# Optimization experiments

Measured on AMD Instinct MI355X. Metric: run time of the kernel, lower is better.

Reference implementation:

```python
import jax, jax.numpy as jnp
import numpy as np

N_EMBD = 1024
N_HEAD = 16
LORA_R = 8
LORA_ALPHA = 16
SCALE = LORA_ALPHA / LORA_R


def lora_linear(x, W, b, A, Bm):
    # loralib: F.linear(x, W, b) + (x @ A.T @ B.T) * scaling
    return x @ W.T + b + ((x @ A.T) @ Bm.T) * SCALE


def setup_inputs() -> dict:
    key = jax.random.key(0)
    ks = jax.random.split(key, 9)
    B, T, C = 4, 2048, N_EMBD
    s_in = 1.0 / np.sqrt(C)
    x = jax.random.normal(ks[0], (B, T, C), dtype=jnp.float32)
    Wqkv = jax.random.normal(ks[1], (3 * C, C), dtype=jnp.float32) * s_in
    bqkv = jnp.zeros((3 * C,), dtype=jnp.float32)
    Aqkv = jax.random.normal(ks[2], (LORA_R, C), dtype=jnp.float32) * s_in
    Bqkv = jnp.zeros((3 * C, LORA_R), dtype=jnp.float32)  # loralib inits B to zero
    Wproj = jax.random.normal(ks[3], (C, C), dtype=jnp.float32) * s_in
    bproj = jnp.zeros((C,), dtype=jnp.float32)
    Aproj = jax.random.normal(ks[4], (LORA_R, C), dtype=jnp.float32) * s_in
    Bproj = jnp.zeros((C, LORA_R), dtype=jnp.float32)
    return {"x": x, "Wqkv": Wqkv, "bqkv": bqkv, "Aqkv": Aqkv, "Bqkv": Bqkv,
            "Wproj": Wproj, "bproj": bproj, "Aproj": Aproj, "Bproj": Bproj}


def reference(x, Wqkv, bqkv, Aqkv, Bqkv, Wproj, bproj, Aproj, Bproj):
    B, T, C = x.shape
    H, D = N_HEAD, C // N_HEAD
    qkv = lora_linear(x, Wqkv, bqkv, Aqkv, Bqkv)  # [B,T,3C]
    q, k, v = jnp.split(qkv, 3, axis=2)
    # [B,T,C] -> [B,H,T,D]
    q = q.reshape(B, T, H, D).transpose(0, 2, 1, 3)
    k = k.reshape(B, T, H, D).transpose(0, 2, 1, 3)
    v = v.reshape(B, T, H, D).transpose(0, 2, 1, 3)
    att = jnp.einsum("bhqd,bhkd->bhqk", q, k) * (1.0 / np.sqrt(D))
    causal = jnp.tril(jnp.ones((T, T), dtype=bool))
    att = jnp.where(causal[None, None], att, jnp.float32(-jnp.inf))
    att = jax.nn.softmax(att, axis=-1)
    out = jnp.einsum("bhqk,bhkd->bhqd", att, v)  # [B,H,T,D]
    out = out.transpose(0, 2, 1, 3).reshape(B, T, C)
    return lora_linear(out, Wproj, bproj, Aproj, Bproj)
```

## Files before the change

kernel.cpp:

```cpp
#include <hip/hip_runtime.h>
#include <hip/hip_bf16.h>

typedef __bf16 bf16_t;
typedef __bf16 bf16x8 __attribute__((ext_vector_type(8)));
typedef __bf16 bf16x4 __attribute__((ext_vector_type(4)));
typedef float  f32x4  __attribute__((ext_vector_type(4)));

#define MFMA_BF16 __builtin_amdgcn_mfma_f32_16x16x32_bf16
#define NEG_BIG  (-3.0e38f)

#if __has_builtin(__builtin_amdgcn_exp2f)
#define EXP2F(x) __builtin_amdgcn_exp2f(x)
#else
#define EXP2F(x) exp2f(x)
#endif

#define SBAR()       __builtin_amdgcn_s_barrier()
#define SCHED0()     __builtin_amdgcn_sched_barrier(0)
#define WAIT_LGKM0() asm volatile("s_waitcnt lgkmcnt(0)" ::: "memory")
#define WAIT_LGKM8() asm volatile("s_waitcnt lgkmcnt(8)" ::: "memory")
#define WAIT_VM0()   asm volatile("s_waitcnt vmcnt(0)" ::: "memory")
#define WAIT_VM4()   asm volatile("s_waitcnt vmcnt(4)" ::: "memory")
#define WAIT_VM6()   asm volatile("s_waitcnt vmcnt(6)" ::: "memory")

__device__ __forceinline__ void load16_lds(const bf16_t* g, bf16_t* l) {
    __builtin_amdgcn_global_load_lds(
        (const __attribute__((address_space(1))) void*)g,
        (__attribute__((address_space(3))) void*)l, 16, 0, 0);
}

__device__ inline bf16x8 ld8(const bf16_t* p) { return *(const bf16x8*)p; }
__device__ inline bf16x8 ld8(const float* p) {
    f32x4 a = *(const f32x4*)p;
    f32x4 b = *(const f32x4*)(p + 4);
    bf16x8 o;
    o[0] = (bf16_t)a[0]; o[1] = (bf16_t)a[1]; o[2] = (bf16_t)a[2]; o[3] = (bf16_t)a[3];
    o[4] = (bf16_t)b[0]; o[5] = (bf16_t)b[1]; o[6] = (bf16_t)b[2]; o[7] = (bf16_t)b[3];
    return o;
}

template <typename TX>
__device__ __forceinline__ void lora_xa_body(
    const TX* __restrict__ X, const float* __restrict__ A,
    float* __restrict__ out, int m, int lane)
{
    const TX* xp = X + (size_t)m * 1024;
    float acc[8];
#pragma unroll
    for (int r = 0; r < 8; r++) acc[r] = 0.f;

#pragma unroll 4
    for (int ci = 0; ci < 16; ci++) {
        int k = ci * 64 + lane;
        float xv = (float)xp[k];
#pragma unroll
        for (int r = 0; r < 8; r++) acc[r] += xv * A[r * 1024 + k];
    }
#pragma unroll
    for (int r = 0; r < 8; r++) {
        float v = acc[r];
        v += __shfl_xor(v, 1);  v += __shfl_xor(v, 2);  v += __shfl_xor(v, 4);
        v += __shfl_xor(v, 8);  v += __shfl_xor(v, 16); v += __shfl_xor(v, 32);
        if (lane == 0) out[m * 8 + r] = v;
    }
}

template <typename TX>
__global__ __launch_bounds__(256) void lora_xa_kernel(
    const TX* __restrict__ X, const float* __restrict__ A,
    float* __restrict__ out)
{
    const int lane = threadIdx.x & 63;
    const int w    = threadIdx.x >> 6;
    const int m    = blockIdx.x * 4 + w;
    lora_xa_body<TX>(X, A, out, m, lane);
}

__global__ __launch_bounds__(256) void prep_kernel(
    const float* __restrict__ x, const float* __restrict__ Wqkv,
    const float* __restrict__ Wproj,
    bf16_t* __restrict__ x16, bf16_t* __restrict__ Wqkv16,
    bf16_t* __restrict__ Wproj16,
    const float* __restrict__ Aqkv, float* __restrict__ xa1)
{
    const int bid = blockIdx.x;
    if (bid < 6144) {
        const float* in; bf16_t* out; size_t off;
        if (bid < 4096)      { in = x;     out = x16;     off = (size_t)bid * 2048; }
        else if (bid < 5632) { in = Wqkv;  out = Wqkv16;  off = (size_t)(bid - 4096) * 2048; }
        else                 { in = Wproj; out = Wproj16; off = (size_t)(bid - 5632) * 2048; }
        size_t i = off + (size_t)threadIdx.x * 8;
        *(bf16x8*)&out[i] = ld8(&in[i]);
    } else {
        const int lane = threadIdx.x & 63;
        const int w    = threadIdx.x >> 6;
        const int m    = (bid - 6144) * 4 + w;
        lora_xa_body<float>(x, Aqkv, xa1, m, lane);
    }
}

__device__ __forceinline__ void gemm_epilogue(
    f32x4 (&acc)[4][4], const float* bias, const float* xA, const float* LB,
    bf16_t* C0, bf16_t* C1, bf16_t* C2, float* Cf,
    int tile_m, int tile_n, int wm, int wn, int c, int g)
{
    const int seg    = tile_n >> 10;
    const int tn_loc = tile_n & 1023;
    bf16_t* Cout = (seg == 0) ? C0 : (seg == 1) ? C1 : C2;

    float biasf[4];
    float lbv[4][8];
#pragma unroll
    for (int j = 0; j < 4; j++) {
        int col = tile_n + wn + j * 16 + c;
        biasf[j] = bias[col];
        f32x4 lb0 = *(const f32x4*)&LB[(size_t)col * 8];
        f32x4 lb1 = *(const f32x4*)&LB[(size_t)col * 8 + 4];
#pragma unroll
        for (int r = 0; r < 4; r++) { lbv[j][r] = lb0[r]; lbv[j][r + 4] = lb1[r]; }
    }
#pragma unroll
    for (int i = 0; i < 4; i++) {
#pragma unroll
        for (int rg = 0; rg < 4; rg++) {
            int row = tile_m + wm + i * 16 + g * 4 + rg;
            f32x4 xa0 = *(const f32x4*)&xA[(size_t)row * 8];
            f32x4 xa1 = *(const f32x4*)&xA[(size_t)row * 8 + 4];
#pragma unroll
            for (int j = 0; j < 4; j++) {
                float lora = xa0[0] * lbv[j][0] + xa0[1] * lbv[j][1] +
                             xa0[2] * lbv[j][2] + xa0[3] * lbv[j][3] +
                             xa1[0] * lbv[j][4] + xa1[1] * lbv[j][5] +
                             xa1[2] * lbv[j][6] + xa1[3] * lbv[j][7];
                float v = acc[i][j][rg] + biasf[j] + 2.0f * lora;
                int lcol = tn_loc + wn + j * 16 + c;
                if (Cf) Cf[(size_t)row * 1024 + lcol] = v;
                else    Cout[(size_t)row * 1024 + lcol] = (bf16_t)v;
            }
        }
    }
}

template <typename TA, typename TW>
__global__ __launch_bounds__(256) void gemm_bias_lora(
    const TA* __restrict__ A, const TW* __restrict__ W,
    const float* __restrict__ bias, const float* __restrict__ xA,
    const float* __restrict__ LB,
    bf16_t* __restrict__ C0, bf16_t* __restrict__ C1, bf16_t* __restrict__ C2,
    float* __restrict__ Cf, int K)
{
    __shared__ __align__(16) bf16_t As[128 * 72];
    __shared__ __align__(16) bf16_t Bs[128 * 72];

    const int t    = threadIdx.x;
    const int lane = t & 63;
    const int w    = t >> 6;
    const int wm   = (w >> 1) * 64;
    const int wn   = (w & 1) * 64;
    const int c    = lane & 15;
    const int g    = lane >> 4;
    const int tile_m = blockIdx.y * 128;
    const int tile_n = blockIdx.x * 128;

    const int srow = t >> 3;
    const int scol = (t & 7) * 8;

    f32x4 acc[4][4];
#pragma unroll
    for (int i = 0; i < 4; i++)
#pragma unroll
        for (int j = 0; j < 4; j++) {
            f32x4 z = {0.f, 0.f, 0.f, 0.f};
            acc[i][j] = z;
        }

    for (int k0 = 0; k0 < K; k0 += 64) {
#pragma unroll
        for (int i = 0; i < 4; i++) {
            int r = srow + i * 32;
            *(bf16x8*)&As[r * 72 + scol] = ld8(&A[(size_t)(tile_m + r) * K + k0 + scol]);
            *(bf16x8*)&Bs[r * 72 + scol] = ld8(&W[(size_t)(tile_n + r) * K + k0 + scol]);
        }
        __syncthreads();

#pragma unroll
        for (int kk = 0; kk < 2; kk++) {
            bf16x8 af[4], bfr[4];
#pragma unroll
            for (int i = 0; i < 4; i++)
                af[i] = *(const bf16x8*)&As[(wm + i * 16 + c) * 72 + kk * 32 + g * 8];
#pragma unroll
            for (int j = 0; j < 4; j++)
                bfr[j] = *(const bf16x8*)&Bs[(wn + j * 16 + c) * 72 + kk * 32 + g * 8];
#pragma unroll
            for (int i = 0; i < 4; i++)
#pragma unroll
                for (int j = 0; j < 4; j++)
                    acc[i][j] = MFMA_BF16(af[i], bfr[j], acc[i][j], 0, 0, 0);
        }
        __syncthreads();
    }
    gemm_epilogue(acc, bias, xA, LB, C0, C1, C2, Cf, tile_m, tile_n, wm, wn, c, g);
}

#define AS_OFF(row, q) ((row) * 64 + (((q) ^ ((row) & 7)) * 8))

__global__ __launch_bounds__(256) void gemm_proj_fused(
    const bf16_t* __restrict__ A, const bf16_t* __restrict__ W,
    const float* __restrict__ bias, const float* __restrict__ Ap,
    const float* __restrict__ LB, float* __restrict__ Cf, int K)
{
    __shared__ __align__(16) bf16_t As[128 * 64];
    __shared__ __align__(16) bf16_t Bs[128 * 64];
    __shared__ __align__(16) bf16_t Ap16[8 * 1032];

    const int t    = threadIdx.x;
    const int lane = t & 63;
    const int w    = t >> 6;
    const int wm   = (w >> 1) * 64;
    const int wn   = (w & 1) * 64;
    const int c    = lane & 15;
    const int g    = lane >> 4;
    const int tile_m = blockIdx.y * 128;
    const int tile_n = blockIdx.x * 128;

    {
        int r = t >> 5;
        int k = (t & 31) * 32;
        const float* src = Ap + (size_t)r * 1024 + k;
        bf16_t* dst = &Ap16[r * 1032 + k];
#pragma unroll
        for (int e = 0; e < 32; e += 8)
            *(bf16x8*)&dst[e] = ld8(&src[e]);
    }

    const int trow = t >> 3;
    const int k8   = (t & 7) ^ (trow & 7);
    const bf16_t* Ab = A + (size_t)tile_m * K + k8 * 8;
    const bf16_t* Wb = W + (size_t)tile_n * K + k8 * 8;

    f32x4 acc[4][4];
#pragma unroll
    for (int i = 0; i < 4; i++)
#pragma unroll
        for (int j = 0; j < 4; j++) {
            f32x4 z = {0.f, 0.f, 0.f, 0.f};
            acc[i][j] = z;
        }
    f32x4 accx[2];
    {
        f32x4 z = {0.f, 0.f, 0.f, 0.f};
        accx[0] = z; accx[1] = z;
    }

    for (int k0 = 0; k0 < K; k0 += 64) {
#pragma unroll
        for (int i = 0; i < 4; i++) {
            int row = i * 32 + trow;
            load16_lds(&Ab[(size_t)row * K + k0], &As[(i * 256 + t) * 8]);
            load16_lds(&Wb[(size_t)row * K + k0], &Bs[(i * 256 + t) * 8]);
        }
        __syncthreads();

#pragma unroll
        for (int kk = 0; kk < 2; kk++) {
            bf16x8 af[4], bfr[4];
#pragma unroll
            for (int i = 0; i < 4; i++)
                af[i] = *(const bf16x8*)&As[AS_OFF(wm + i * 16 + c, kk * 4 + g)];
#pragma unroll
            for (int j = 0; j < 4; j++)
                bfr[j] = *(const bf16x8*)&Bs[AS_OFF(wn + j * 16 + c, kk * 4 + g)];
#pragma unroll
            for (int i = 0; i < 4; i++)
#pragma unroll
                for (int j = 0; j < 4; j++)
                    acc[i][j] = MFMA_BF16(af[i], bfr[j], acc[i][j], 0, 0, 0);
            bf16x8 apf = *(const bf16x8*)&Ap16[(c & 7) * 1032 + k0 + kk * 32 + g * 8];
#pragma unroll
            for (int fi = 0; fi < 2; fi++) {
                bf16x8 xf = *(const bf16x8*)&As[AS_OFF(w * 32 + fi * 16 + c, kk * 4 + g)];
                accx[fi] = MFMA_BF16(xf, apf, accx[fi], 0, 0, 0);
            }
        }
        __syncthreads();
    }

    float* xa2l = (float*)As;
    if (c < 8) {
#pragma unroll
        for (int fi = 0; fi < 2; fi++)
#pragma unroll
            for (int rg = 0; rg < 4; rg++)
                xa2l[(w * 32 + fi * 16 + g * 4 + rg) * 8 + c] = accx[fi][rg];
    }
    __syncthreads();

    float biasf[4];
    float lbv[4][8];
#pragma unroll
    for (int j = 0; j < 4; j++) {
        int col = tile_n + wn + j * 16 + c;
        biasf[j] = bias[col];
        f32x4 lb0 = *(const f32x4*)&LB[(size_t)col * 8];
        f32x4 lb1 = *(const f32x4*)&LB[(size_t)col * 8 + 4];
#pragma unroll
        for (int r = 0; r < 4; r++) { lbv[j][r] = lb0[r]; lbv[j][r + 4] = lb1[r]; }
    }
#pragma unroll
    for (int i = 0; i < 4; i++) {
#pragma unroll
        for (int rg = 0; rg < 4; rg++) {
            int rloc = wm + i * 16 + g * 4 + rg;
            int row  = tile_m + rloc;
            f32x4 xa0 = *(const f32x4*)&xa2l[rloc * 8];
            f32x4 xa1 = *(const f32x4*)&xa2l[rloc * 8 + 4];
#pragma unroll
            for (int j = 0; j < 4; j++) {
                float lora = xa0[0] * lbv[j][0] + xa0[1] * lbv[j][1] +
                             xa0[2] * lbv[j][2] + xa0[3] * lbv[j][3] +
                             xa1[0] * lbv[j][4] + xa1[1] * lbv[j][5] +
                             xa1[2] * lbv[j][6] + xa1[3] * lbv[j][7];
                float v = acc[i][j][rg] + biasf[j] + 2.0f * lora;
                Cf[(size_t)row * 1024 + tile_n + wn + j * 16 + c] = v;
            }
        }
    }
}

__global__ __launch_bounds__(512, 2) void gemm_256(
    const bf16_t* __restrict__ A, const bf16_t* __restrict__ W,
    const float* __restrict__ bias, const float* __restrict__ xA,
    const float* __restrict__ LB,
    bf16_t* __restrict__ C0, bf16_t* __restrict__ C1, bf16_t* __restrict__ C2,
    float* __restrict__ Cf, int K, int ntn)
{
    __shared__ __align__(16) bf16_t As[4][8192];
    __shared__ __align__(16) bf16_t Bs[4][8192];

    const int t    = threadIdx.x;
    const int lane = t & 63;
    const int w    = t >> 6;
    const int c    = lane & 15;
    const int g    = lane >> 4;

    const int nwg = gridDim.x;
    const int cpx = nwg >> 3;
    const int bid = blockIdx.x;
    const int swz = (bid & 7) * cpx + (bid >> 3);
    const int tile_m = (swz / ntn) * 256;
    const int tile_n = (swz % ntn) * 256;

    const int wm  = (w >> 2) * 128;
    const int wn  = (w & 3) * 64;
    const int ha  = w >> 2;
    const int hb  = wn >> 7;
    const int wnl = wn & 127;

    int aoffs[8][2], boffs[4][2];
#pragma unroll
    for (int il = 0; il < 8; il++) {
        int rl = il * 16 + c;
#pragma unroll
        for (int ks = 0; ks < 2; ks++)
            aoffs[il][ks] = rl * 64 + (((ks * 4 + g) ^ (rl & 7)) * 8);
    }
#pragma unroll
    for (int j2 = 0; j2 < 4; j2++) {
        int rl = wnl + j2 * 16 + c;
#pragma unroll
        for (int ks = 0; ks < 2; ks++)
            boffs[j2][ks] = rl * 64 + (((ks * 4 + g) ^ (rl & 7)) * 8);
    }

    const int trow = t >> 3;
    const int qq   = (t & 7) ^ (trow & 7);
    const bf16_t* aO = A + (size_t)(tile_m + trow) * K + qq * 8;
    const bf16_t* wO = W + (size_t)(tile_n + trow) * K + qq * 8;
    const size_t rK64 = (size_t)64 * K;

#define STAGE_A(T, h) do {                                                         \
    load16_lds(aO + (size_t)(h) * 128 * K + (size_t)(T) * 64,                      \
               &As[((T) & 1) * 2 + (h)][t * 8]);                                   \
    load16_lds(aO + (size_t)(h) * 128 * K + rK64 + (size_t)(T) * 64,               \
               &As[((T) & 1) * 2 + (h)][4096 + t * 8]); } while (0)
#define STAGE_B(T, h) do {                                                         \
    load16_lds(wO + (size_t)(h) * 128 * K + (size_t)(T) * 64,                      \
               &Bs[((T) & 1) * 2 + (h)][t * 8]);                                   \
    load16_lds(wO + (size_t)(h) * 128 * K + rK64 + (size_t)(T) * 64,               \
               &Bs[((T) & 1) * 2 + (h)][4096 + t * 8]); } while (0)

    f32x4 acc[8][4];
#pragma unroll
    for (int i = 0; i < 8; i++)
#pragma unroll
        for (int j2 = 0; j2 < 4; j2++) {
            f32x4 z = {0.f, 0.f, 0.f, 0.f};
            acc[i][j2] = z;
        }

    const int NT = K >> 6;

    STAGE_B(0, 0); STAGE_B(0, 1); STAGE_A(0, 0); STAGE_A(0, 1);
    WAIT_VM4();
    STAGE_B(1, 0); STAGE_B(1, 1); STAGE_A(1, 0);
    WAIT_VM6();
    SBAR();

    for (int j = 0; j < NT; j++) {
        const bf16_t* Ab = &As[(j & 1) * 2 + ha][0];
        const bf16_t* Bb = &Bs[(j & 1) * 2 + hb][0];
        bf16x8 bfr[4][2], af0[4], af1[4];

#pragma unroll
        for (int j2 = 0; j2 < 4; j2++) {
            bfr[j2][0] = *(const bf16x8*)&Bb[boffs[j2][0]];
            bfr[j2][1] = *(const bf16x8*)&Bb[boffs[j2][1]];
        }
#pragma unroll
        for (int i = 0; i < 4; i++) af0[i] = *(const bf16x8*)&Ab[aoffs[i][0]];
        if (j + 1 < NT) STAGE_A(j + 1, 1);
        WAIT_LGKM8();
        SBAR();
        WAIT_LGKM0();
        SCHED0();
        __builtin_amdgcn_s_setprio(1);
#pragma unroll
        for (int i = 0; i < 4; i++)
#pragma unroll
            for (int j2 = 0; j2 < 4; j2++)
                acc[i][j2] = MFMA_BF16(af0[i], bfr[j2][0], acc[i][j2], 0, 0, 0);
        __builtin_amdgcn_s_setprio(0);
        SBAR();

#pragma unroll
        for (int i = 0; i < 4; i++) af1[i] = *(const bf16x8*)&Ab[aoffs[i + 4][0]];
        if (j + 2 < NT) STAGE_B(j + 2, 0);
        SBAR();
        WAIT_LGKM0();
        SCHED0();
        __builtin_amdgcn_s_setprio(1);
#pragma unroll
        for (int i = 0; i < 4; i++)
#pragma unroll
            for (int j2 = 0; j2 < 4; j2++)
                acc[4 + i][j2] = MFMA_BF16(af1[i], bfr[j2][0], acc[4 + i][j2], 0, 0, 0);
        __builtin_amdgcn_s_setprio(0);
        SBAR();

#pragma unroll
        for (int i = 0; i < 4; i++) af0[i] = *(const bf16x8*)&Ab[aoffs[i][1]];
#pragma unroll
        for (int i = 0; i < 4; i++) af1[i] = *(const bf16x8*)&Ab[aoffs[i + 4][1]];
        if (j + 2 < NT) STAGE_B(j + 2, 1);
        SBAR();
        WAIT_LGKM0();
        SCHED0();
        __builtin_amdgcn_s_setprio(1);
#pragma unroll
        for (int i = 0; i < 4; i++)
#pragma unroll
            for (int j2 = 0; j2 < 4; j2++)
                acc[i][j2] = MFMA_BF16(af0[i], bfr[j2][1], acc[i][j2], 0, 0, 0);
        __builtin_amdgcn_s_setprio(0);
        SBAR();

        if (j + 2 < NT) STAGE_A(j + 2, 0);
        SBAR();
        __builtin_amdgcn_s_setprio(1);
#pragma unroll
        for (int i = 0; i < 4; i++)
#pragma unroll
            for (int j2 = 0; j2 < 4; j2++)
                acc[4 + i][j2] = MFMA_BF16(af1[i], bfr[j2][1], acc[4 + i][j2], 0, 0, 0);
        __builtin_amdgcn_s_setprio(0);
        if (j < NT - 2) WAIT_VM6(); else WAIT_VM0();
        SBAR();
    }
#undef STAGE_A
#undef STAGE_B

    const int seg    = tile_n >> 10;
    const int tn_loc = tile_n & 1023;
    bf16_t* Cout = (seg == 0) ? C0 : (seg == 1) ? C1 : C2;

    float biasf[4];
    float lbv[4][8];
#pragma unroll
    for (int j2 = 0; j2 < 4; j2++) {
        int col = tile_n + wn + j2 * 16 + c;
        biasf[j2] = bias[col];
        f32x4 lb0 = *(const f32x4*)&LB[(size_t)col * 8];
        f32x4 lb1 = *(const f32x4*)&LB[(size_t)col * 8 + 4];
#pragma unroll
        for (int r = 0; r < 4; r++) { lbv[j2][r] = lb0[r]; lbv[j2][r + 4] = lb1[r]; }
    }
#pragma unroll
    for (int i = 0; i < 8; i++) {
#pragma unroll
        for (int rg = 0; rg < 4; rg++) {
            int row = tile_m + wm + i * 16 + g * 4 + rg;
            f32x4 xa0 = *(const f32x4*)&xA[(size_t)row * 8];
            f32x4 xa1 = *(const f32x4*)&xA[(size_t)row * 8 + 4];
#pragma unroll
            for (int j2 = 0; j2 < 4; j2++) {
                float lora = xa0[0] * lbv[j2][0] + xa0[1] * lbv[j2][1] +
                             xa0[2] * lbv[j2][2] + xa0[3] * lbv[j2][3] +
                             xa1[0] * lbv[j2][4] + xa1[1] * lbv[j2][5] +
                             xa1[2] * lbv[j2][6] + xa1[3] * lbv[j2][7];
                float v = acc[i][j2][rg] + biasf[j2] + 2.0f * lora;
                int lcol = tn_loc + wn + j2 * 16 + c;
                if (Cf) Cf[(size_t)row * 1024 + lcol] = v;
                else    Cout[(size_t)row * 1024 + lcol] = (bf16_t)v;
            }
        }
    }
}

#define VT_IDX(d, kv) ((d) * 72 + ((d) >> 4) * 16 + (kv))
#define PS_IDX(q, kv) ((q) * 72 + ((q) >> 2) * 8 + (kv))
#define PW_REGION 1168

__global__ __launch_bounds__(256, 2) void attn_kernel(
    bf16_t* __restrict__ Q, const bf16_t* __restrict__ Kg,
    const bf16_t* __restrict__ Vg)
{
    __shared__ __align__(16) bf16_t Ks[64 * 72];
    __shared__ __align__(16) bf16_t Vt[64 * 72 + 64];
    __shared__ __align__(16) bf16_t Ps[8 * PW_REGION];

    const int t    = threadIdx.x;
    const int lane = t & 63;
    const int w    = t >> 6;
    const int c    = lane & 15;
    const int g    = lane >> 4;

    const int id = blockIdx.x;
    const int qb = 15 - (id >> 6);
    const int h  = id & 15;
    const int b  = (id >> 4) & 3;
    const int q0 = qb * 128;
    const size_t base = (size_t)b * 2048 * 1024;
    const int last = 2 * qb + 1;

    bf16x8 qfA[2], qfB[2];
    {
        const bf16_t* qpA = Q + base + (size_t)(q0 + w * 16 + c) * 1024 + h * 64;
        qfA[0] = *(const bf16x8*)&qpA[g * 8];
        qfA[1] = *(const bf16x8*)&qpA[32 + g * 8];
        const bf16_t* qpB = qpA + (size_t)64 * 1024;
        qfB[0] = *(const bf16x8*)&qpB[g * 8];
        qfB[1] = *(const bf16x8*)&qpB[32 + g * 8];
    }

    bf16x8 ones;
#pragma unroll
    for (int e = 0; e < 8; e++) ones[e] = (bf16_t)1.0f;

    f32x4 accA[4], accB[4];
#pragma unroll
    for (int jd = 0; jd < 4; jd++) {
        f32x4 z = {0.f, 0.f, 0.f, 0.f};
        accA[jd] = z; accB[jd] = z;
    }
    f32x4 lA = {0.f, 0.f, 0.f, 0.f};
    f32x4 lB = {0.f, 0.f, 0.f, 0.f};
    float mA = NEG_BIG, mB = NEG_BIG;

    const int sr = t >> 2;
    const int sc = (t & 3) * 16;
    const int vtbase = VT_IDX(sc, sr);

    bf16x8 kr0, kr1, vr0, vr1;
    {
        const bf16_t* kp = Kg + base + (size_t)sr * 1024 + h * 64 + sc;
        kr0 = *(const bf16x8*)&kp[0];
        kr1 = *(const bf16x8*)&kp[8];
        const bf16_t* vp = Vg + base + (size_t)sr * 1024 + h * 64 + sc;
        vr0 = *(const bf16x8*)&vp[0];
        vr1 = *(const bf16x8*)&vp[8];
    }

    bf16_t* PwA = &Ps[(w * 2 + 0) * PW_REGION];
    bf16_t* PwB = &Ps[(w * 2 + 1) * PW_REGION];
    const float SCL = 0.125f * 1.44269504088896f;

    for (int kt = 0; kt <= last; kt++) {
        if (kt > 0) __syncthreads();
        *(bf16x8*)&Ks[sr * 72 + sc]     = kr0;
        *(bf16x8*)&Ks[sr * 72 + sc + 8] = kr1;
#pragma unroll
        for (int e = 0; e < 8; e++) Vt[vtbase + e * 72]       = vr0[e];
#pragma unroll
        for (int e = 0; e < 8; e++) Vt[vtbase + (e + 8) * 72] = vr1[e];
        __syncthreads();

        if (kt < last) {
            const bf16_t* kp = Kg + base + (size_t)((kt + 1) * 64 + sr) * 1024 + h * 64 + sc;
            kr0 = *(const bf16x8*)&kp[0];
            kr1 = *(const bf16x8*)&kp[8];
            const bf16_t* vp = Vg + base + (size_t)((kt + 1) * 64 + sr) * 1024 + h * 64 + sc;
            vr0 = *(const bf16x8*)&vp[0];
            vr1 = *(const bf16x8*)&vp[8];
        }

        const bool doA = (kt <= 2 * qb);

        f32x4 sA[4], sB[4];
#pragma unroll
        for (int j = 0; j < 4; j++) {
            f32x4 z = {0.f, 0.f, 0.f, 0.f};
            sA[j] = z; sB[j] = z;
        }
#pragma unroll
        for (int kk = 0; kk < 2; kk++) {
            bf16x8 kf[4];
#pragma unroll
            for (int j = 0; j < 4; j++)
                kf[j] = *(const bf16x8*)&Ks[(j * 16 + c) * 72 + kk * 32 + g * 8];
            if (doA) {
#pragma unroll
                for (int j = 0; j < 4; j++)
                    sA[j] = MFMA_BF16(kf[j], qfA[kk], sA[j], 0, 0, 0);
            }
#pragma unroll
            for (int j = 0; j < 4; j++)
                sB[j] = MFMA_BF16(kf[j], qfB[kk], sB[j], 0, 0, 0);
        }

        if (doA) {
#pragma unroll
            for (int j = 0; j < 4; j++)
#pragma unroll
                for (int r = 0; r < 4; r++) sA[j][r] *= SCL;
            if (kt == 2 * qb) {
#pragma unroll
                for (int j = 0; j < 4; j++)
#pragma unroll
                    for (int r = 0; r < 4; r++)
                        if (j * 16 + g * 4 + r > w * 16 + c) sA[j][r] = NEG_BIG;
            }
            float mx;
            {
                float a0 = fmaxf(fmaxf(sA[0][0], sA[0][1]), fmaxf(sA[0][2], sA[0][3]));
                float a1 = fmaxf(fmaxf(sA[1][0], sA[1][1]), fmaxf(sA[1][2], sA[1][3]));
                float a2 = fmaxf(fmaxf(sA[2][0], sA[2][1]), fmaxf(sA[2][2], sA[2][3]));
                float a3 = fmaxf(fmaxf(sA[3][0], sA[3][1]), fmaxf(sA[3][2], sA[3][3]));
                mx = fmaxf(fmaxf(a0, a1), fmaxf(a2, a3));
                mx = fmaxf(mx, __shfl_xor(mx, 16));
                mx = fmaxf(mx, __shfl_xor(mx, 32));
            }
            if (!__all(mx <= mA + 8.0f)) {
                float mnew  = fmaxf(mA, mx);
                float alpha = EXP2F(mA - mnew);
                mA = mnew;
#pragma unroll
                for (int jd = 0; jd < 4; jd++)
#pragma unroll
                    for (int r = 0; r < 4; r++) accA[jd][r] *= alpha;
                lA[0] *= alpha;
            }
#pragma unroll
            for (int j = 0; j < 4; j++)
#pragma unroll
                for (int r = 0; r < 4; r++) sA[j][r] = EXP2F(sA[j][r] - mA);
#pragma unroll
            for (int j = 0; j < 4; j++) {
                bf16x4 pk;
#pragma unroll
                for (int r = 0; r < 4; r++) pk[r] = (bf16_t)sA[j][r];
                *(bf16x4*)&PwA[PS_IDX(c, j * 16 + g * 4)] = pk;
            }
        }

        {
#pragma unroll
            for (int j = 0; j < 4; j++)
#pragma unroll
                for (int r = 0; r < 4; r++) sB[j][r] *= SCL;
            if (kt == last) {
#pragma unroll
                for (int j = 0; j < 4; j++)
#pragma unroll
                    for (int r = 0; r < 4; r++)
                        if (j * 16 + g * 4 + r > w * 16 + c) sB[j][r] = NEG_BIG;
            }
            float mx;
            {
                float a0 = fmaxf(fmaxf(sB[0][0], sB[0][1]), fmaxf(sB[0][2], sB[0][3]));
                float a1 = fmaxf(fmaxf(sB[1][0], sB[1][1]), fmaxf(sB[1][2], sB[1][3]));
                float a2 = fmaxf(fmaxf(sB[2][0], sB[2][1]), fmaxf(sB[2][2], sB[2][3]));
                float a3 = fmaxf(fmaxf(sB[3][0], sB[3][1]), fmaxf(sB[3][2], sB[3][3]));
                mx = fmaxf(fmaxf(a0, a1), fmaxf(a2, a3));
                mx = fmaxf(mx, __shfl_xor(mx, 16));
                mx = fmaxf(mx, __shfl_xor(mx, 32));
            }
            if (!__all(mx <= mB + 8.0f)) {
                float mnew  = fmaxf(mB, mx);
                float alpha = EXP2F(mB - mnew);
                mB = mnew;
#pragma unroll
                for (int jd = 0; jd < 4; jd++)
#pragma unroll
                    for (int r = 0; r < 4; r++) accB[jd][r] *= alpha;
                lB[0] *= alpha;
            }
#pragma unroll
            for (int j = 0; j < 4; j++)
#pragma unroll
                for (int r = 0; r < 4; r++) sB[j][r] = EXP2F(sB[j][r] - mB);
#pragma unroll
            for (int j = 0; j < 4; j++) {
                bf16x4 pk;
#pragma unroll
                for (int r = 0; r < 4; r++) pk[r] = (bf16_t)sB[j][r];
                *(bf16x4*)&PwB[PS_IDX(c, j * 16 + g * 4)] = pk;
            }
        }

#pragma unroll
        for (int kkv = 0; kkv < 2; kkv++) {
            bf16x8 vf[4];
#pragma unroll
            for (int jd = 0; jd < 4; jd++)
                vf[jd] = *(const bf16x8*)&Vt[VT_IDX(jd * 16 + c, kkv * 32 + g * 8)];
            if (doA) {
                bf16x8 pfA = *(const bf16x8*)&PwA[PS_IDX(c, kkv * 32 + g * 8)];
#pragma unroll
                for (int jd = 0; jd < 4; jd++)
                    accA[jd] = MFMA_BF16(vf[jd], pfA, accA[jd], 0, 0, 0);
                lA = MFMA_BF16(ones, pfA, lA, 0, 0, 0);
            }
            bf16x8 pfB = *(const bf16x8*)&PwB[PS_IDX(c, kkv * 32 + g * 8)];
#pragma unroll
            for (int jd = 0; jd < 4; jd++)
                accB[jd] = MFMA_BF16(vf[jd], pfB, accB[jd], 0, 0, 0);
            lB = MFMA_BF16(ones, pfB, lB, 0, 0, 0);
        }
    }

    {
        float rl = 1.0f / lA[0];
        bf16_t* op = Q + base + (size_t)(q0 + w * 16 + c) * 1024 + h * 64;
#pragma unroll
        for (int jd = 0; jd < 4; jd++) {
            bf16x4 o4;
#pragma unroll
            for (int r = 0; r < 4; r++) o4[r] = (bf16_t)(accA[jd][r] * rl);
            *(bf16x4*)&op[jd * 16 + g * 4] = o4;
        }
    }
    {
        float rl = 1.0f / lB[0];
        bf16_t* op = Q + base + (size_t)(q0 + 64 + w * 16 + c) * 1024 + h * 64;
#pragma unroll
        for (int jd = 0; jd < 4; jd++) {
            bf16x4 o4;
#pragma unroll
            for (int r = 0; r < 4; r++) o4[r] = (bf16_t)(accB[jd][r] * rl);
            *(bf16x4*)&op[jd * 16 + g * 4] = o4;
        }
    }
}

extern "C" void kernel_launch(void* const* d_in, const int* in_sizes, int n_in,
                              void* d_out, int out_size, void* d_ws, size_t ws_size,
                              hipStream_t stream) {
    const float* x     = (const float*)d_in[0];
    const float* Wqkv  = (const float*)d_in[1];
    const float* bqkv  = (const float*)d_in[2];
    const float* Aqkv  = (const float*)d_in[3];
    const float* Bqkv  = (const float*)d_in[4];
    const float* Wproj = (const float*)d_in[5];
    const float* bproj = (const float*)d_in[6];
    const float* Aproj = (const float*)d_in[7];
    const float* Bproj = (const float*)d_in[8];
    float* out = (float*)d_out;

    char* ws = (char*)d_ws;
    const bool big = ws_size >= (size_t)(72.5 * 1024 * 1024) + 65536;

    if (big) {
        float*  xa1    = (float*)ws;
        bf16_t* x16    = (bf16_t*)(ws + 524288);
        bf16_t* Wqkv16 = x16 + (size_t)8192 * 1024;
        bf16_t* Wproj16= Wqkv16 + (size_t)3072 * 1024;
        bf16_t* Qfull  = Wproj16 + (size_t)1024 * 1024;
        bf16_t* Kfull  = Qfull + (size_t)8192 * 1024;
        bf16_t* Vfull  = Kfull + (size_t)8192 * 1024;

        prep_kernel<<<8192, 256, 0, stream>>>(
            x, Wqkv, Wproj, x16, Wqkv16, Wproj16, Aqkv, xa1);

        gemm_256<<<384, 512, 0, stream>>>(
            x16, Wqkv16, bqkv, xa1, Bqkv, Qfull, Kfull, Vfull, nullptr, 1024, 12);

        attn_kernel<<<1024, 256, 0, stream>>>(Qfull, Kfull, Vfull);

        gemm_proj_fused<<<dim3(8, 64), 256, 0, stream>>>(
            Qfull, Wproj16, bproj, Aproj, Bproj, out, 1024);
    } else {
        float*  xa1   = (float*)ws;
        float*  xa2   = (float*)(ws + 262144);
        bf16_t* Qfull = (bf16_t*)(ws + 524288);
        bf16_t* Kfull = Qfull + (size_t)8192 * 1024;
        bf16_t* Vfull = Kfull + (size_t)8192 * 1024;

        lora_xa_kernel<float><<<2048, 256, 0, stream>>>(x, Aqkv, xa1);
        gemm_bias_lora<float, float><<<dim3(24, 64), 256, 0, stream>>>(
            x, Wqkv, bqkv, xa1, Bqkv, Qfull, Kfull, Vfull, nullptr, 1024);
        attn_kernel<<<1024, 256, 0, stream>>>(Qfull, Kfull, Vfull);
        lora_xa_kernel<bf16_t><<<2048, 256, 0, stream>>>(Qfull, Aproj, xa2);
        gemm_bias_lora<bf16_t, float><<<dim3(8, 64), 256, 0, stream>>>(
            Qfull, Wproj, bproj, xa2, Bproj,
            nullptr, nullptr, nullptr, out, 1024);
    }
}
```

Before: 301.1 us.

## Fuse LoRA x@A^T computation into QKV GEMM main loop via extra MFMAs

The QKV GEMM now converts the LoRA A matrix to bf16 in shared memory and computes x@A^T for its tile's rows with two extra MFMAs per half-step, reusing the A tiles already staged in LDS. The result is written to LDS for the epilogue instead of being read from a precomputed global buffer. This lets the prep kernel launch fewer blocks because it no longer has to compute xa1. The cost is about 16KB of extra LDS, additional MFMA and LDS-read work in every block (computed redundantly across the 12 column tiles), and x@A^T now accumulates at bf16 input precision.

```diff
diff --git a/kernel.cpp b/kernel.cpp
--- a/kernel.cpp
+++ b/kernel.cpp
@@ -330,13 +330,14 @@
 
 __global__ __launch_bounds__(512, 2) void gemm_256(
     const bf16_t* __restrict__ A, const bf16_t* __restrict__ W,
-    const float* __restrict__ bias, const float* __restrict__ xA,
+    const float* __restrict__ bias, const float* __restrict__ Aq,
     const float* __restrict__ LB,
     bf16_t* __restrict__ C0, bf16_t* __restrict__ C1, bf16_t* __restrict__ C2,
     float* __restrict__ Cf, int K, int ntn)
 {
     __shared__ __align__(16) bf16_t As[4][8192];
     __shared__ __align__(16) bf16_t Bs[4][8192];
+    __shared__ __align__(16) bf16_t Aq16[8 * 1032];
 
     const int t    = threadIdx.x;
     const int lane = t & 63;
@@ -357,6 +358,15 @@
     const int hb  = wn >> 7;
     const int wnl = wn & 127;
 
+    {
+        int r = t >> 6;
+        int k = (t & 63) * 16;
+        const float* src = Aq + (size_t)r * 1024 + k;
+        bf16_t* dst = &Aq16[r * 1032 + k];
+        *(bf16x8*)&dst[0] = ld8(&src[0]);
+        *(bf16x8*)&dst[8] = ld8(&src[8]);
+    }
+
     int aoffs[8][2], boffs[4][2];
 #pragma unroll
     for (int il = 0; il < 8; il++) {
@@ -371,6 +381,16 @@
 #pragma unroll
         for (int ks = 0; ks < 2; ks++)
             boffs[j2][ks] = rl * 64 + (((ks * 4 + g) ^ (rl & 7)) * 8);
+    }
+
+    const int xrow0 = (w & 3) * 32;
+    int xoffs[2][2];
+#pragma unroll
+    for (int fi = 0; fi < 2; fi++) {
+        int rl = xrow0 + fi * 16 + c;
+#pragma unroll
+        for (int ks = 0; ks < 2; ks++)
+            xoffs[fi][ks] = rl * 64 + (((ks * 4 + g) ^ (rl & 7)) * 8);
     }
 
     const int trow = t >> 3;
@@ -398,12 +418,18 @@
             f32x4 z = {0.f, 0.f, 0.f, 0.f};
             acc[i][j2] = z;
         }
+    f32x4 accx[2];
+    {
+        f32x4 z = {0.f, 0.f, 0.f, 0.f};
+        accx[0] = z; accx[1] = z;
+    }
 
     const int NT = K >> 6;
 
     STAGE_B(0, 0); STAGE_B(0, 1); STAGE_A(0, 0); STAGE_A(0, 1);
     WAIT_VM4();
     STAGE_B(1, 0); STAGE_B(1, 1); STAGE_A(1, 0);
+    WAIT_LGKM0();
     WAIT_VM6();
     SBAR();
 
@@ -411,6 +437,7 @@
         const bf16_t* Ab = &As[(j & 1) * 2 + ha][0];
         const bf16_t* Bb = &Bs[(j & 1) * 2 + hb][0];
         bf16x8 bfr[4][2], af0[4], af1[4];
+        bf16x8 xf0a, xf1a, xf0b, xf1b, apf0, apf1;
 
 #pragma unroll
         for (int j2 = 0; j2 < 4; j2++) {
@@ -435,6 +462,9 @@
 
 #pragma unroll
         for (int i = 0; i < 4; i++) af1[i] = *(const bf16x8*)&Ab[aoffs[i + 4][0]];
+        xf0a = *(const bf16x8*)&Ab[xoffs[0][0]];
+        xf1a = *(const bf16x8*)&Ab[xoffs[1][0]];
+        apf0 = *(const bf16x8*)&Aq16[(c & 7) * 1032 + j * 64 + g * 8];
         if (j + 2 < NT) STAGE_B(j + 2, 0);
         SBAR();
         WAIT_LGKM0();
@@ -445,6 +475,8 @@
 #pragma unroll
             for (int j2 = 0; j2 < 4; j2++)
                 acc[4 + i][j2] = MFMA_BF16(af1[i], bfr[j2][0], acc[4 + i][j2], 0, 0, 0);
+        accx[0] = MFMA_BF16(xf0a, apf0, accx[0], 0, 0, 0);
+        accx[1] = MFMA_BF16(xf1a, apf0, accx[1], 0, 0, 0);
         __builtin_amdgcn_s_setprio(0);
         SBAR();
 
@@ -452,6 +484,9 @@
         for (int i = 0; i < 4; i++) af0[i] = *(const bf16x8*)&Ab[aoffs[i][1]];
 #pragma unroll
         for (int i = 0; i < 4; i++) af1[i] = *(const bf16x8*)&Ab[aoffs[i + 4][1]];
+        xf0b = *(const bf16x8*)&Ab[xoffs[0][1]];
+        xf1b = *(const bf16x8*)&Ab[xoffs[1][1]];
+        apf1 = *(const bf16x8*)&Aq16[(c & 7) * 1032 + j * 64 + 32 + g * 8];
         if (j + 2 < NT) STAGE_B(j + 2, 1);
         SBAR();
         WAIT_LGKM0();
@@ -473,12 +508,24 @@
 #pragma unroll
             for (int j2 = 0; j2 < 4; j2++)
                 acc[4 + i][j2] = MFMA_BF16(af1[i], bfr[j2][1], acc[4 + i][j2], 0, 0, 0);
+        accx[0] = MFMA_BF16(xf0b, apf1, accx[0], 0, 0, 0);
+        accx[1] = MFMA_BF16(xf1b, apf1, accx[1], 0, 0, 0);
         __builtin_amdgcn_s_setprio(0);
         if (j < NT - 2) WAIT_VM6(); else WAIT_VM0();
         SBAR();
     }
 #undef STAGE_A
 #undef STAGE_B
+
+    float* xl = (float*)&As[0][0];
+    if (c < 8) {
+#pragma unroll
+        for (int fi = 0; fi < 2; fi++)
+#pragma unroll
+            for (int rg = 0; rg < 4; rg++)
+                xl[(ha * 128 + xrow0 + fi * 16 + g * 4 + rg) * 8 + c] = accx[fi][rg];
+    }
+    __syncthreads();
 
     const int seg    = tile_n >> 10;
     const int tn_loc = tile_n & 1023;
@@ -499,9 +546,10 @@
     for (int i = 0; i < 8; i++) {
 #pragma unroll
         for (int rg = 0; rg < 4; rg++) {
-            int row = tile_m + wm + i * 16 + g * 4 + rg;
-            f32x4 xa0 = *(const f32x4*)&xA[(size_t)row * 8];
-            f32x4 xa1 = *(const f32x4*)&xA[(size_t)row * 8 + 4];
+            int rloc = wm + i * 16 + g * 4 + rg;
+            int row  = tile_m + rloc;
+            f32x4 xa0 = *(const f32x4*)&xl[rloc * 8];
+            f32x4 xa1 = *(const f32x4*)&xl[rloc * 8 + 4];
 #pragma unroll
             for (int j2 = 0; j2 < 4; j2++) {
                 float lora = xa0[0] * lbv[j2][0] + xa0[1] * lbv[j2][1] +
@@ -789,11 +837,11 @@
         bf16_t* Kfull  = Qfull + (size_t)8192 * 1024;
         bf16_t* Vfull  = Kfull + (size_t)8192 * 1024;
 
-        prep_kernel<<<8192, 256, 0, stream>>>(
+        prep_kernel<<<6144, 256, 0, stream>>>(
             x, Wqkv, Wproj, x16, Wqkv16, Wproj16, Aqkv, xa1);
 
         gemm_256<<<384, 512, 0, stream>>>(
-            x16, Wqkv16, bqkv, xa1, Bqkv, Qfull, Kfull, Vfull, nullptr, 1024, 12);
+            x16, Wqkv16, bqkv, Aqkv, Bqkv, Qfull, Kfull, Vfull, nullptr, 1024, 12);
 
         attn_kernel<<<1024, 256, 0, stream>>>(Qfull, Kfull, Vfull);
 
```

New measurement: 289.1 us. 4.0% less time.
